# Kernel optimization log

Measured on AMD Instinct MI355X. Metric: run time of the kernel, lower is better.

## Reference

```python
import jax
jax.config.update("jax_enable_x64", True)  # hash primes * indices overflow int32
import jax.numpy as jnp
import numpy as np

HASH_SIZE = 2 ** 19
DIM = 32
CELL_SIZE = 1.0
N = 2_000_000
PRIME_X = 73856093
PRIME_Y = 19349663


def setup_inputs() -> dict:
    key = jax.random.key(0)
    k_pos, k_tab = jax.random.split(key)
    # uniform [0,1) scaled to cover many grid cells (cell_size = 1.0)
    positions = jax.random.uniform(k_pos, (N, 2), dtype=jnp.float32) * 4096.0
    # each slot initialized like torch.randn(dim) * 0.01
    table = jax.random.normal(k_tab, (HASH_SIZE, DIM), dtype=jnp.float32) * 0.01
    return {"positions": positions, "table": table}


def _hash_positions(positions):
    # quantize to integer cell coords, then spatial hash (batch_lookup math)
    ij = jnp.floor(positions / CELL_SIZE).astype(jnp.int64)  # [N,2]
    ix, iy = ij[:, 0], ij[:, 1]
    return jnp.mod(jnp.bitwise_xor(ix * PRIME_X, iy * PRIME_Y), HASH_SIZE)


def reference(positions, table):
    hashed = _hash_positions(positions)          # [N] int64 in [0, HASH_SIZE)
    return jnp.take(table, hashed, axis=0)       # [N, DIM] gather
```

## Files before the change

kernel.cpp:

```cpp
#include <hip/hip_runtime.h>


#define HASH_MASK ((1u << 19) - 1u)
#define SLICE_SHIFT 15
#define NSLICE 16
#define BLOCK 512
#define CHUNK 512
#define CAP 128
#define RSTRIDE 9

typedef float vfloat2 __attribute__((ext_vector_type(2)));
typedef float vfloat4 __attribute__((ext_vector_type(4)));

__global__ __launch_bounds__(BLOCK) void HashGrid2D_37383395344981_kernel(
    const vfloat2* __restrict__ pos,
    const vfloat4* __restrict__ table,
    vfloat4* __restrict__ out,
    int n)
{
    __shared__ vfloat4 buf[CHUNK * RSTRIDE];
    __shared__ unsigned list[2][CAP];
    __shared__ unsigned cnt[2];

    const int tid = threadIdx.x;
    const int r0 = blockIdx.x * CHUNK;
    const int r = r0 + tid;

    unsigned h = 0xFFFFFFFFu;
    if (r < n) {
        vfloat2 p = __builtin_nontemporal_load(&pos[r]);
        unsigned ix = (unsigned)(int)floorf(p.x);
        unsigned iy = (unsigned)(int)floorf(p.y);
        h = ((ix * 73856093u) ^ (iy * 19349663u)) & HASH_MASK;
    }

    if (tid < 2) cnt[tid] = 0u;
    __syncthreads();

    for (unsigned s = 0; s < NSLICE; ++s) {
        const unsigned b = s & 1u;

        if ((h >> SLICE_SHIFT) == s) {
            unsigned idx = atomicAdd(&cnt[b], 1u);
            if (idx < CAP) {
                list[b][idx] = (h << 9) | (unsigned)tid;
            } else {
                const vfloat4* trow = table + (size_t)h * 8;
                vfloat4* lrow = buf + (size_t)tid * RSTRIDE;
#pragma unroll
                for (int c = 0; c < 8; ++c) lrow[c] = trow[c];
            }
        }
        __syncthreads();

        if (tid == 0) cnt[b ^ 1u] = 0u;
        unsigned m = cnt[b]; if (m > CAP) m = CAP;
        for (unsigned i = tid; i < m; i += BLOCK) {
            unsigned e = list[b][i];
            unsigned hh = e >> 9;
            unsigned lr = e & 511u;
            const vfloat4* trow = table + (size_t)hh * 8;
            vfloat4 v0 = trow[0], v1 = trow[1], v2 = trow[2], v3 = trow[3];
            vfloat4 v4 = trow[4], v5 = trow[5], v6 = trow[6], v7 = trow[7];
            vfloat4* lrow = buf + (size_t)lr * RSTRIDE;
            lrow[0] = v0; lrow[1] = v1; lrow[2] = v2; lrow[3] = v3;
            lrow[4] = v4; lrow[5] = v5; lrow[6] = v6; lrow[7] = v7;
        }
        __syncthreads();
    }

    int nrow = n - r0; if (nrow > CHUNK) nrow = CHUNK;
    int nf4 = nrow * 8;
    vfloat4* obase = out + (size_t)r0 * 8;
    for (int i = tid; i < nf4; i += BLOCK) {
        int row = i >> 3, c = i & 7;
        __builtin_nontemporal_store(buf[(size_t)row * RSTRIDE + c], &obase[i]);
    }
}

extern "C" void kernel_launch(void* const* d_in, const int* in_sizes, int n_in,
                              void* d_out, int out_size, void* d_ws, size_t ws_size,
                              hipStream_t stream) {
    const vfloat2* pos   = (const vfloat2*)d_in[0];
    const vfloat4* table = (const vfloat4*)d_in[1];
    vfloat4* out = (vfloat4*)d_out;

    int n = in_sizes[0] / 2;
    int grid = (n + CHUNK - 1) / CHUNK;

    HashGrid2D_37383395344981_kernel<<<grid, BLOCK, 0, stream>>>(pos, table, out, n);
}
```

Before: 397.3 us.

## Replace per-slice sync loop with block counting sort and cooperative row gather

Removes the 16-iteration slice loop, which needed two block barriers per slice and left most threads idle. Rows are now bucketed by hash slice with a shared-memory counting sort: an atomic rank per slice, then a prefix sum done by one thread. All 512 threads then gather in one pass, with 8 threads cooperating on each 128-byte table row so the loads are coalesced. The cost is a short serial prefix sum, an extra perm array in shared memory, and that loads from different slices are no longer separated in time, which may loosen any cache locality the slicing gave.

```diff
diff --git a/kernel.cpp b/kernel.cpp
--- a/kernel.cpp
+++ b/kernel.cpp
@@ -6,7 +6,6 @@
 #define NSLICE 16
 #define BLOCK 512
 #define CHUNK 512
-#define CAP 128
 #define RSTRIDE 9
 
 typedef float vfloat2 __attribute__((ext_vector_type(2)));
@@ -19,62 +18,59 @@
     int n)
 {
     __shared__ vfloat4 buf[CHUNK * RSTRIDE];
-    __shared__ unsigned list[2][CAP];
-    __shared__ unsigned cnt[2];
+    __shared__ unsigned cnt[NSLICE];
+    __shared__ unsigned sbase[NSLICE];
+    __shared__ unsigned perm[CHUNK];
 
     const int tid = threadIdx.x;
     const int r0 = blockIdx.x * CHUNK;
     const int r = r0 + tid;
+    const bool valid = (r < n);
 
-    unsigned h = 0xFFFFFFFFu;
-    if (r < n) {
+    if (tid < NSLICE) cnt[tid] = 0u;
+    __syncthreads();
+
+    unsigned h = 0u, rank = 0u;
+    if (valid) {
         vfloat2 p = __builtin_nontemporal_load(&pos[r]);
         unsigned ix = (unsigned)(int)floorf(p.x);
         unsigned iy = (unsigned)(int)floorf(p.y);
         h = ((ix * 73856093u) ^ (iy * 19349663u)) & HASH_MASK;
+        rank = atomicAdd(&cnt[h >> SLICE_SHIFT], 1u);
     }
-
-    if (tid < 2) cnt[tid] = 0u;
     __syncthreads();
 
-    for (unsigned s = 0; s < NSLICE; ++s) {
-        const unsigned b = s & 1u;
+    if (tid == 0) {
+        unsigned acc = 0u;
+#pragma unroll
+        for (int s = 0; s < NSLICE; ++s) { sbase[s] = acc; acc += cnt[s]; }
+    }
+    __syncthreads();
 
-        if ((h >> SLICE_SHIFT) == s) {
-            unsigned idx = atomicAdd(&cnt[b], 1u);
-            if (idx < CAP) {
-                list[b][idx] = (h << 9) | (unsigned)tid;
-            } else {
-                const vfloat4* trow = table + (size_t)h * 8;
-                vfloat4* lrow = buf + (size_t)tid * RSTRIDE;
-#pragma unroll
-                for (int c = 0; c < 8; ++c) lrow[c] = trow[c];
-            }
-        }
-        __syncthreads();
+    if (valid) perm[sbase[h >> SLICE_SHIFT] + rank] = (h << 9) | (unsigned)tid;
+    __syncthreads();
 
-        if (tid == 0) cnt[b ^ 1u] = 0u;
-        unsigned m = cnt[b]; if (m > CAP) m = CAP;
-        for (unsigned i = tid; i < m; i += BLOCK) {
-            unsigned e = list[b][i];
+    const int nrow = (n - r0 < CHUNK) ? (n - r0) : CHUNK;
+    const int c = tid & 7;
+    const int ri = tid >> 3;
+#pragma unroll 8
+    for (int j = 0; j < CHUNK / 64; ++j) {
+        int i = ri + 64 * j;
+        if (i < nrow) {
+            unsigned e = perm[i];
             unsigned hh = e >> 9;
             unsigned lr = e & 511u;
-            const vfloat4* trow = table + (size_t)hh * 8;
-            vfloat4 v0 = trow[0], v1 = trow[1], v2 = trow[2], v3 = trow[3];
-            vfloat4 v4 = trow[4], v5 = trow[5], v6 = trow[6], v7 = trow[7];
-            vfloat4* lrow = buf + (size_t)lr * RSTRIDE;
-            lrow[0] = v0; lrow[1] = v1; lrow[2] = v2; lrow[3] = v3;
-            lrow[4] = v4; lrow[5] = v5; lrow[6] = v6; lrow[7] = v7;
+            vfloat4 v = table[(size_t)hh * 8 + c];
+            buf[(size_t)lr * RSTRIDE + c] = v;
         }
-        __syncthreads();
     }
+    __syncthreads();
 
-    int nrow = n - r0; if (nrow > CHUNK) nrow = CHUNK;
-    int nf4 = nrow * 8;
+    const int nf4 = nrow * 8;
     vfloat4* obase = out + (size_t)r0 * 8;
     for (int i = tid; i < nf4; i += BLOCK) {
-        int row = i >> 3, c = i & 7;
-        __builtin_nontemporal_store(buf[(size_t)row * RSTRIDE + c], &obase[i]);
+        int row = i >> 3, cc = i & 7;
+        __builtin_nontemporal_store(buf[(size_t)row * RSTRIDE + cc], &obase[i]);
     }
 }
 
```

After: 335.8 us. 1.18x faster.
